# Kernel tuning notes

Hardware: AMD Instinct MI355X
Metric: run time of the kernel (lower is better)

The kernel has to match this reference:

```python
import jax, jax.numpy as jnp
import numpy as np
import math

DIM = 1536
N_HEADS = 12
HEAD_DIM = DIM // N_HEADS  # 128
C = HEAD_DIM // 2          # 64 complex rotation channels
CT = C - 2 * (C // 3)      # 22 temporal channels
CH = C // 3                # 21 height channels
CW = C // 3                # 21 width channels
F, H, W = 3, 30, 52        # video latent grid -> S = 4680
S = F * H * W
B = 1
EPS = 1e-6
NEG = -1e30


def _rope_angles(max_pos, sizes):
    # Wan-style rope_params per axis: theta_j = 10000^(-j/m) for m complex dims
    parts = []
    pos = jnp.arange(max_pos, dtype=jnp.float32)
    for m in sizes:
        inv = 10000.0 ** (-jnp.arange(m, dtype=jnp.float32) / m)
        parts.append(pos[:, None] * inv[None, :])
    return jnp.concatenate(parts, axis=-1)  # [max_pos, C]


def setup_inputs() -> dict:
    key = jax.random.key(0)
    ks = jax.random.split(key, 6)
    sc = 0.02
    inp = {
        'x': jax.random.normal(ks[0], (B, S, DIM), jnp.float32),
        'seq_lens': jnp.array([S], dtype=jnp.int32),
        'grid_sizes': jnp.array([[F, H, W]], dtype=jnp.int32),
        'freqs': _rope_angles(1024, [CT, CH, CW]),  # [1024, 64] rotation angles
        'Wq': jax.random.normal(ks[1], (DIM, DIM), jnp.float32) * sc,
        'bq': jnp.zeros((DIM,), jnp.float32),
        'Wk': jax.random.normal(ks[2], (DIM, DIM), jnp.float32) * sc,
        'bk': jnp.zeros((DIM,), jnp.float32),
        'Wv': jax.random.normal(ks[3], (DIM, DIM), jnp.float32) * sc,
        'bv': jnp.zeros((DIM,), jnp.float32),
        'Wo': jax.random.normal(ks[4], (DIM, DIM), jnp.float32) * sc,
        'bo': jnp.zeros((DIM,), jnp.float32),
        'gq': jnp.ones((DIM,), jnp.float32),
        'gk': jnp.ones((DIM,), jnp.float32),
    }
    return inp


def _rmsnorm(x, g):
    return x * jax.lax.rsqrt(jnp.mean(x * x, axis=-1, keepdims=True) + EPS) * g


def _apply_rope(x, grid_sizes, freqs):
    # x: [B, S, n, d]; rotate consecutive pairs by 3D (t,h,w) factorized angles.
    b, s, n, d = x.shape
    f = grid_sizes[0, 0]
    h = grid_sizes[0, 1]
    w = grid_sizes[0, 2]
    pos = jnp.arange(s)
    t_idx = pos // (h * w)
    y_idx = (pos % (h * w)) // w
    x_idx = pos % w
    ang = jnp.concatenate([
        freqs[t_idx, :CT],
        freqs[y_idx, CT:CT + CH],
        freqs[x_idx, CT + CH:],
    ], axis=-1)  # [S, C]
    cos = jnp.cos(ang)[None, :, None, :]  # [1, S, 1, C]
    sin = jnp.sin(ang)[None, :, None, :]
    xp = x.reshape(b, s, n, d // 2, 2)
    xr, xi = xp[..., 0], xp[..., 1]
    out_r = xr * cos - xi * sin
    out_i = xr * sin + xi * cos
    return jnp.stack([out_r, out_i], axis=-1).reshape(b, s, n, d)


def reference(x, seq_lens, grid_sizes, freqs, Wq, bq, Wk, bk, Wv, bv, Wo, bo, gq, gk):
    b, s, _ = x.shape
    n, d = N_HEADS, HEAD_DIM
    q = _rmsnorm(x @ Wq.T + bq, gq).reshape(b, s, n, d)
    k = _rmsnorm(x @ Wk.T + bk, gk).reshape(b, s, n, d)
    v = (x @ Wv.T + bv).reshape(b, s, n, d)

    rq = _apply_rope(q, grid_sizes, freqs)
    rk = _apply_rope(k, grid_sizes, freqs)

    # frame-level block-causal mask (block_mask in the original flex_attention)
    frame_seqlen = grid_sizes[0, 1] * grid_sizes[0, 2]
    frame_id = jnp.arange(s) // frame_seqlen
    allowed = frame_id[:, None] >= frame_id[None, :]  # [S, S]

    scale = 1.0 / math.sqrt(d)
    scores = jnp.einsum('bqnd,bknd->bnqk', rq, rk) * scale
    scores = jnp.where(allowed[None, None], scores, NEG)
    attn = jax.nn.softmax(scores, axis=-1)
    out = jnp.einsum('bnqk,bknd->bqnd', attn, v).reshape(b, s, n * d)
    return out @ Wo.T + bo
```

## Files before the change

### kernel.cpp

```cpp
#include <hip/hip_runtime.h>
#include <hip/hip_bf16.h>
#include <math.h>
#include <stdint.h>

#define S_LEN 4680
#define DIMSZ 1536
#define NH    12
#define HD    128
#define FRAME 1560
#define SP    4736
#define SQPAD 4736

typedef _Float16 f16;
typedef _Float16 f16x8 __attribute__((ext_vector_type(8)));
typedef _Float16 f16x4 __attribute__((ext_vector_type(4)));
typedef __fp16   fp16x2 __attribute__((ext_vector_type(2)));
typedef float    f32x4 __attribute__((ext_vector_type(4)));

__device__ __forceinline__ void async16(const void* g, void* l) {
    __builtin_amdgcn_global_load_lds((const __attribute__((address_space(1))) void*)g,
                                     (__attribute__((address_space(3))) void*)l, 16, 0, 0);
}

union PkCast { fp16x2 v; int i; };
union FragCast { int w[4]; f16x8 v; };

__global__ __launch_bounds__(256) void cast_f32_f16(const float* __restrict__ src,
                                                    f16* __restrict__ dst, int n4) {
    int i = blockIdx.x * 256 + threadIdx.x;
    if (i < n4) {
        float4 v = ((const float4*)src)[i];
        f16x4 h;
        h[0] = (f16)v.x; h[1] = (f16)v.y; h[2] = (f16)v.z; h[3] = (f16)v.w;
        ((f16x4*)dst)[i] = h;
    }
}

__global__ __launch_bounds__(256) void gemm_lds(const f16* __restrict__ A,
                                                const f16* __restrict__ B,
                                                const float* __restrict__ bias,
                                                float* __restrict__ C) {
    __shared__ __align__(16) f16 Al[128 * 64];
    __shared__ __align__(16) f16 Bl[128 * 64];
    int tid = threadIdx.x;
    int lane = tid & 63, wv = tid >> 6;
    int l16 = lane & 15, quad = lane >> 4;
    int wr = (wv >> 1) * 64, wc = (wv & 1) * 64;
    int m0 = blockIdx.x * 128, n0 = blockIdx.y * 128;

    f32x4 acc[4][4] = {};

    for (int kb = 0; kb < DIMSZ; kb += 64) {
        __syncthreads();
#pragma unroll
        for (int j = 0; j < 4; j++) {
            int s = j * 256 + wv * 64 + lane;
            int r = s >> 3, cc = s & 7;
            const f16* src = A + (size_t)min(m0 + r, S_LEN - 1) * DIMSZ + kb + ((cc ^ (r & 7)) << 3);
            async16(src, (char*)Al + (j * 4096 + wv * 1024));
        }
#pragma unroll
        for (int j = 0; j < 4; j++) {
            int s = j * 256 + wv * 64 + lane;
            int r = s >> 3, cc = s & 7;
            const f16* src = B + (size_t)(n0 + r) * DIMSZ + kb + ((cc ^ (r & 7)) << 3);
            async16(src, (char*)Bl + (j * 4096 + wv * 1024));
        }
        __builtin_amdgcn_s_waitcnt(0x0f70);
        __syncthreads();

#pragma unroll
        for (int kc = 0; kc < 2; kc++) {
            f16x8 af[4], bf[4];
#pragma unroll
            for (int i = 0; i < 4; i++) {
                int ar = wr + i * 16 + l16;
                af[i] = *(const f16x8*)((const char*)Al + ar * 128 + (((kc * 4 + quad) ^ (ar & 7)) << 4));
                int br = wc + i * 16 + l16;
                bf[i] = *(const f16x8*)((const char*)Bl + br * 128 + (((kc * 4 + quad) ^ (br & 7)) << 4));
            }
#pragma unroll
            for (int mi = 0; mi < 4; mi++)
#pragma unroll
                for (int ni = 0; ni < 4; ni++)
                    acc[mi][ni] = __builtin_amdgcn_mfma_f32_16x16x32_f16(af[mi], bf[ni], acc[mi][ni], 0, 0, 0);
        }
    }

#pragma unroll
    for (int mi = 0; mi < 4; mi++)
#pragma unroll
        for (int ni = 0; ni < 4; ni++) {
            int col = n0 + wc + ni * 16 + l16;
            float bv = bias[col];
#pragma unroll
            for (int r = 0; r < 4; r++) {
                int row = m0 + wr + mi * 16 + quad * 4 + r;
                if (row < S_LEN) C[(size_t)row * DIMSZ + col] = acc[mi][ni][r] + bv;
            }
        }
}

__global__ __launch_bounds__(256) void gemm_ldsvt(const f16* __restrict__ A,
                                                  const f16* __restrict__ B,
                                                  const float* __restrict__ bias,
                                                  f16* __restrict__ Vt) {
    __shared__ __align__(16) f16 Al[128 * 64];
    __shared__ __align__(16) f16 Bl[128 * 64];
    int tid = threadIdx.x;
    int lane = tid & 63, wv = tid >> 6;
    int l16 = lane & 15, quad = lane >> 4;
    int wr = (wv >> 1) * 64, wc = (wv & 1) * 64;
    int m0 = blockIdx.x * 128, n0 = blockIdx.y * 128;

    f32x4 acc[4][4] = {};

    for (int kb = 0; kb < DIMSZ; kb += 64) {
        __syncthreads();
#pragma unroll
        for (int j = 0; j < 4; j++) {
            int s = j * 256 + wv * 64 + lane;
            int r = s >> 3, cc = s & 7;
            const f16* src = A + (size_t)min(m0 + r, S_LEN - 1) * DIMSZ + kb + ((cc ^ (r & 7)) << 3);
            async16(src, (char*)Al + (j * 4096 + wv * 1024));
        }
#pragma unroll
        for (int j = 0; j < 4; j++) {
            int s = j * 256 + wv * 64 + lane;
            int r = s >> 3, cc = s & 7;
            const f16* src = B + (size_t)(n0 + r) * DIMSZ + kb + ((cc ^ (r & 7)) << 3);
            async16(src, (char*)Bl + (j * 4096 + wv * 1024));
        }
        __builtin_amdgcn_s_waitcnt(0x0f70);
        __syncthreads();

#pragma unroll
        for (int kc = 0; kc < 2; kc++) {
            f16x8 af[4], bf[4];
#pragma unroll
            for (int i = 0; i < 4; i++) {
                int ar = wr + i * 16 + l16;
                af[i] = *(const f16x8*)((const char*)Al + ar * 128 + (((kc * 4 + quad) ^ (ar & 7)) << 4));
                int br = wc + i * 16 + l16;
                bf[i] = *(const f16x8*)((const char*)Bl + br * 128 + (((kc * 4 + quad) ^ (br & 7)) << 4));
            }
#pragma unroll
            for (int mi = 0; mi < 4; mi++)
#pragma unroll
                for (int ni = 0; ni < 4; ni++)
                    acc[mi][ni] = __builtin_amdgcn_mfma_f32_16x16x32_f16(af[mi], bf[ni], acc[mi][ni], 0, 0, 0);
        }
    }

#pragma unroll
    for (int mi = 0; mi < 4; mi++)
#pragma unroll
        for (int ni = 0; ni < 4; ni++) {
            int col  = n0 + wc + ni * 16 + l16;
            int base = m0 + wr + mi * 16 + quad * 4;
            if (base < S_LEN) {
                float bv = bias[col];
                f16x4 h;
#pragma unroll
                for (int r = 0; r < 4; r++) h[r] = (f16)(acc[mi][ni][r] + bv);
                *(f16x4*)(Vt + (size_t)col * SP + base) = h;
            }
        }
}

__global__ __launch_bounds__(256) void norm_rope(const float* __restrict__ pre,
                                                 const float* __restrict__ g,
                                                 const float* __restrict__ freqs,
                                                 f16* __restrict__ dst) {
    int s = blockIdx.x;
    int t = threadIdx.x;
    const float* row = pre + (size_t)s * DIMSZ;

    float v[6];
    float ss = 0.f;
#pragma unroll
    for (int i = 0; i < 6; i++) { v[i] = row[t * 6 + i]; ss += v[i] * v[i]; }
#pragma unroll
    for (int off = 32; off; off >>= 1) ss += __shfl_xor(ss, off);
    __shared__ float red[4];
    if ((t & 63) == 0) red[t >> 6] = ss;
    __syncthreads();
    float tot = red[0] + red[1] + red[2] + red[3];
    float rms = rsqrtf(tot * (1.0f / DIMSZ) + 1e-6f);

    int tpos = s / FRAME;
    int rem  = s % FRAME;
    int ypos = rem / 52;
    int xpos = s % 52;

#pragma unroll
    for (int u = 0; u < 3; u++) {
        int c = t * 6 + u * 2;
        int head = c >> 7;
        int d = c & 127;
        int j = d >> 1;
        int idx = (j < 22) ? tpos : ((j < 43) ? ypos : xpos);
        float ang = freqs[idx * 64 + j];
        float sn, cs;
        __sincosf(ang, &sn, &cs);
        float vr = v[u * 2]     * rms * g[c];
        float vi = v[u * 2 + 1] * rms * g[c + 1];
        f16* o = dst + ((size_t)head * S_LEN + s) * HD + d;
        o[0] = (f16)(vr * cs - vi * sn);
        o[1] = (f16)(vr * sn + vi * cs);
    }
}

__global__ __launch_bounds__(256) void attn_part(const f16* __restrict__ Q,
                                                 const f16* __restrict__ K,
                                                 const f16* __restrict__ Vt,
                                                 f16* __restrict__ Opart,
                                                 float* __restrict__ lpart) {
    int bx = blockIdx.x, head = blockIdx.y;
    int t, c;
    if (bx < 12)      { t = bx;                 c = 0; }
    else if (bx < 36) { t = 12 + (bx - 12) / 2; c = (bx - 12) & 1; }
    else              { t = 24 + (bx - 36) / 3; c = (bx - 36) % 3; }

    int tid = threadIdx.x;
    int lane = tid & 63, wv = tid >> 6;
    int l16 = lane & 15, quad = lane >> 4;
    int qbase = t * 128 + wv * 32;

    __shared__ __align__(16) char smem[128 * 136 * 2];
    f16* Klds = (f16*)smem;
    f16* Vlds = (f16*)(smem + 16384);
    f16* obuf = (f16*)smem;

    const f16* Qh = Q  + (size_t)head * S_LEN * HD;
    const f16* Kh = K  + (size_t)head * S_LEN * HD;
    const f16* Vh = Vt + (size_t)head * HD * SP;

    f16x8 aq[2][4];
    int lim[2];
    int c0 = c * FRAME, cend = c0 + FRAME;
#pragma unroll
    for (int qt = 0; qt < 2; qt++) {
        int qr = min(qbase + qt * 16 + l16, S_LEN - 1);
        const f16* Qp = Qh + (size_t)qr * HD + quad * 8;
#pragma unroll
        for (int kc = 0; kc < 4; kc++)
            aq[qt][kc] = (*(const f16x8*)(Qp + kc * 32)) * (f16)0.08838834764831845f;
        lim[qt] = min((qr / FRAME + 1) * FRAME, cend);
    }

    f32x4 oacc[2][8] = {};
    float lp[2] = {0.f, 0.f};

    int losel = ((quad & 1) * 2) * 16 + l16;
    int hisel = losel + 16;
    bool upper = (quad & 2) != 0;

    for (int it = 0; it < 25; it++) {
        int kb = c0 + it * 64;
        __syncthreads();
#pragma unroll
        for (int i = 0; i < 4; i++) {
            int s  = i * 4 + wv;
            int ch = s * 64 + lane;
            int row = ch >> 4;
            int cc  = (ch & 15) ^ (row & 15);
            async16(Kh + (size_t)min(kb + row, S_LEN - 1) * HD + cc * 8,
                    (char*)Klds + s * 1024);
        }
#pragma unroll
        for (int i = 0; i < 4; i++) {
            int s  = i * 4 + wv;
            int ch = s * 64 + lane;
            int vr = ch >> 3;
            int cc = (ch & 7) ^ (vr & 7);
            async16(Vh + (size_t)vr * SP + kb + cc * 8,
                    (char*)Vlds + s * 1024);
        }
        __builtin_amdgcn_s_waitcnt(0x0f70);
        __syncthreads();

        f32x4 sc[2][4] = {};
#pragma unroll
        for (int kt = 0; kt < 4; kt++) {
            int krow = kt * 16 + l16;
#pragma unroll
            for (int kc = 0; kc < 4; kc++) {
                f16x8 kf = *(const f16x8*)((const char*)Klds + krow * 256 +
                                           (((kc * 4 + quad) ^ l16) << 4));
                sc[0][kt] = __builtin_amdgcn_mfma_f32_16x16x32_f16(kf, aq[0][kc], sc[0][kt], 0, 0, 0);
                sc[1][kt] = __builtin_amdgcn_mfma_f32_16x16x32_f16(kf, aq[1][kc], sc[1][kt], 0, 0, 0);
            }
        }

        int dw[2][4][2];
#pragma unroll
        for (int qt = 0; qt < 2; qt++)
#pragma unroll
            for (int kt = 0; kt < 4; kt++) {
                int keyb = kb + kt * 16 + quad * 4;
#pragma unroll
                for (int u = 0; u < 2; u++) {
                    float p0 = (keyb + 2 * u     < lim[qt]) ? __expf(sc[qt][kt][2 * u])     : 0.f;
                    float p1 = (keyb + 2 * u + 1 < lim[qt]) ? __expf(sc[qt][kt][2 * u + 1]) : 0.f;
                    lp[qt] += p0 + p1;
                    PkCast pk; pk.v = __builtin_amdgcn_cvt_pkrtz(p0, p1);
                    dw[qt][kt][u] = pk.i;
                }
            }

        f16x8 pb[2][2];
#pragma unroll
        for (int qt = 0; qt < 2; qt++)
#pragma unroll
            for (int b0 = 0; b0 < 2; b0++) {
                int a0 = __shfl(dw[qt][2 * b0][0],     losel);
                int a1 = __shfl(dw[qt][2 * b0][1],     losel);
                int a2 = __shfl(dw[qt][2 * b0][0],     hisel);
                int a3 = __shfl(dw[qt][2 * b0][1],     hisel);
                int b0w = __shfl(dw[qt][2 * b0 + 1][0], losel);
                int b1w = __shfl(dw[qt][2 * b0 + 1][1], losel);
                int b2w = __shfl(dw[qt][2 * b0 + 1][0], hisel);
                int b3w = __shfl(dw[qt][2 * b0 + 1][1], hisel);
                FragCast fc;
                fc.w[0] = upper ? b0w : a0;
                fc.w[1] = upper ? b1w : a1;
                fc.w[2] = upper ? b2w : a2;
                fc.w[3] = upper ? b3w : a3;
                pb[qt][b0] = fc.v;
            }

#pragma unroll
        for (int vn = 0; vn < 8; vn++) {
            int vrow = vn * 16 + l16;
            f16x8 v0 = *(const f16x8*)((const char*)Vlds + vrow * 128 + (((quad)     ^ (vrow & 7)) << 4));
            f16x8 v1 = *(const f16x8*)((const char*)Vlds + vrow * 128 + (((4 + quad) ^ (vrow & 7)) << 4));
#pragma unroll
            for (int qt = 0; qt < 2; qt++) {
                oacc[qt][vn] = __builtin_amdgcn_mfma_f32_16x16x32_f16(v0, pb[qt][0], oacc[qt][vn], 0, 0, 0);
                oacc[qt][vn] = __builtin_amdgcn_mfma_f32_16x16x32_f16(v1, pb[qt][1], oacc[qt][vn], 0, 0, 0);
            }
        }
    }

    float inv[2];
#pragma unroll
    for (int qt = 0; qt < 2; qt++) {
        float l = lp[qt];
        l += __shfl_xor(l, 16);
        l += __shfl_xor(l, 32);
        lp[qt] = l;
        inv[qt] = 1.f / l;
    }

    __syncthreads();
#pragma unroll
    for (int qt = 0; qt < 2; qt++) {
        int qloc = wv * 32 + qt * 16 + l16;
#pragma unroll
        for (int vn = 0; vn < 8; vn++) {
            f16x4 h;
#pragma unroll
            for (int r = 0; r < 4; r++) h[r] = (f16)(oacc[qt][vn][r] * inv[qt]);
            *(f16x4*)(obuf + qloc * 136 + vn * 16 + quad * 4) = h;
        }
        if (quad == 0) {
            int row = qbase + qt * 16 + l16;
            lpart[(size_t)(c * NH + head) * SQPAD + row] = lp[qt];
        }
    }
    __syncthreads();

    int qloc = tid >> 1, hh = tid & 1;
    size_t obase = ((size_t)(c * NH + head) * SQPAD + t * 128 + qloc) * HD;
#pragma unroll
    for (int p = 0; p < 8; p++) {
        int d = hh * 64 + p * 8;
        f16x8 o = *(const f16x8*)(obuf + qloc * 136 + d);
        *(f16x8*)(Opart + obase + d) = o;
    }
}

__global__ __launch_bounds__(256) void combine(const f16* __restrict__ Opart,
                                               const float* __restrict__ lpart,
                                               f16* __restrict__ AO) {
    int gid = blockIdx.x * 256 + threadIdx.x;
    if (gid >= S_LEN * NH * 16) return;
    int dc = gid & 15;
    int head = (gid >> 4) % NH;
    int q = gid / (NH * 16);
    int tt = q >> 7;
    int qlast = min(tt * 128 + 127, S_LEN - 1);
    int nf = qlast / FRAME + 1;

    float sum[8] = {};
    float ls = 0.f;
    for (int c = 0; c < nf; c++) {
        float l = lpart[(size_t)(c * NH + head) * SQPAD + q];
        if (l > 0.f) {
            f16x8 o = *(const f16x8*)(Opart + ((size_t)(c * NH + head) * SQPAD + q) * HD + dc * 8);
#pragma unroll
            for (int j = 0; j < 8; j++) sum[j] += (float)o[j] * l;
            ls += l;
        }
    }
    float invl = 1.f / ls;
    f16x8 r;
#pragma unroll
    for (int j = 0; j < 8; j++) r[j] = (f16)(sum[j] * invl);
    *(f16x8*)(AO + (size_t)q * DIMSZ + head * HD + dc * 8) = r;
}

extern "C" void kernel_launch(void* const* d_in, const int* in_sizes, int n_in,
                              void* d_out, int out_size, void* d_ws, size_t ws_size,
                              hipStream_t stream) {
    const float* x     = (const float*)d_in[0];
    const float* freqs = (const float*)d_in[3];
    const float* Wq = (const float*)d_in[4];
    const float* bq = (const float*)d_in[5];
    const float* Wk = (const float*)d_in[6];
    const float* bk = (const float*)d_in[7];
    const float* Wv = (const float*)d_in[8];
    const float* bv = (const float*)d_in[9];
    const float* Wo = (const float*)d_in[10];
    const float* bo = (const float*)d_in[11];
    const float* gq = (const float*)d_in[12];
    const float* gk = (const float*)d_in[13];
    float* out = (float*)d_out;

    char* ws = (char*)d_ws;
    const size_t SZ_XH = (size_t)S_LEN * DIMSZ * 2;
    const size_t SZ_W  = (size_t)DIMSZ * DIMSZ * 2;
    const size_t SZ_VT = (size_t)NH * HD * SP * 2;
    const size_t SZ_OP = (size_t)3 * NH * SQPAD * HD * 2;

    size_t off = 0;
    f16* xh  = (f16*)(ws + off); off += SZ_XH;
    f16* wqh = (f16*)(ws + off); off += SZ_W;
    f16* wkh = (f16*)(ws + off); off += SZ_W;
    f16* wvh = (f16*)(ws + off); off += SZ_W;
    f16* woh = (f16*)(ws + off); off += SZ_W;
    f16* Qb  = (f16*)(ws + off); off += SZ_XH;
    f16* Kb  = (f16*)(ws + off); off += SZ_XH;
    f16* Vtb = (f16*)(ws + off); off += SZ_VT;
    f16* AO  = (f16*)(ws + off); off += SZ_XH;
    float* pre   = (float*)(ws + off);
    f16*   Opart = (f16*)(ws + off);
    float* lpart = (float*)(ws + off + SZ_OP);

    const int nX4 = (S_LEN * DIMSZ) / 4;
    const int nW4 = (DIMSZ * DIMSZ) / 4;

    cast_f32_f16<<<nX4 / 256, 256, 0, stream>>>(x,  xh,  nX4);
    cast_f32_f16<<<nW4 / 256, 256, 0, stream>>>(Wq, wqh, nW4);
    cast_f32_f16<<<nW4 / 256, 256, 0, stream>>>(Wk, wkh, nW4);
    cast_f32_f16<<<nW4 / 256, 256, 0, stream>>>(Wv, wvh, nW4);
    cast_f32_f16<<<nW4 / 256, 256, 0, stream>>>(Wo, woh, nW4);

    dim3 ggrid(37, 12);

    gemm_lds<<<ggrid, 256, 0, stream>>>(xh, wqh, bq, pre);
    norm_rope<<<S_LEN, 256, 0, stream>>>(pre, gq, freqs, Qb);
    gemm_lds<<<ggrid, 256, 0, stream>>>(xh, wkh, bk, pre);
    norm_rope<<<S_LEN, 256, 0, stream>>>(pre, gk, freqs, Kb);
    gemm_ldsvt<<<ggrid, 256, 0, stream>>>(xh, wvh, bv, Vtb);

    attn_part<<<dim3(75, 12), 256, 0, stream>>>(Qb, Kb, Vtb, Opart, lpart);
    combine<<<(S_LEN * NH * 16) / 256, 256, 0, stream>>>(Opart, lpart, AO);

    gemm_lds<<<ggrid, 256, 0, stream>>>(AO, woh, bo, out);
}
```

Before: 567.1 us.

## Fuse QKV projections, panelize Q/K/V layout, and rewrite attention with 32x32 MFMA

Merges the five cast kernels into one launch and the three QKV GEMMs into a single z-batched launch. Pre-norm Q/K are stored in fp16 instead of fp32, and Q/K/V are written in a 64-row panel layout so attention can load contiguous 16 KB tiles. The attention kernel now uses 128-thread blocks with 32x32x16 MFMA, permlane32 swaps for the P fragment, and masking only on boundary tiles. This cuts launch count, intermediate traffic and attention instruction overhead, at the cost of extra fp16 rounding before RMSNorm and a larger, more complex kernel.

```diff
diff --git a/kernel.cpp b/kernel.cpp
--- a/kernel.cpp
+++ b/kernel.cpp
@@ -8,14 +8,18 @@
 #define NH    12
 #define HD    128
 #define FRAME 1560
-#define SP    4736
+#define NGRP  74
 #define SQPAD 4736
+#define PANH  (NGRP * 8192)
 
 typedef _Float16 f16;
 typedef _Float16 f16x8 __attribute__((ext_vector_type(8)));
 typedef _Float16 f16x4 __attribute__((ext_vector_type(4)));
+typedef _Float16 f16x2 __attribute__((ext_vector_type(2)));
 typedef __fp16   fp16x2 __attribute__((ext_vector_type(2)));
-typedef float    f32x4 __attribute__((ext_vector_type(4)));
+typedef float    f32x4  __attribute__((ext_vector_type(4)));
+typedef float    f32x16 __attribute__((ext_vector_type(16)));
+typedef int      v2i    __attribute__((ext_vector_type(2)));
 
 __device__ __forceinline__ void async16(const void* g, void* l) {
     __builtin_amdgcn_global_load_lds((const __attribute__((address_space(1))) void*)g,
@@ -25,15 +29,390 @@
 union PkCast { fp16x2 v; int i; };
 union FragCast { int w[4]; f16x8 v; };
 
-__global__ __launch_bounds__(256) void cast_f32_f16(const float* __restrict__ src,
-                                                    f16* __restrict__ dst, int n4) {
+__global__ __launch_bounds__(256) void cast_all(const float* __restrict__ x,
+                                                const float* __restrict__ wq,
+                                                const float* __restrict__ wk,
+                                                const float* __restrict__ wv,
+                                                const float* __restrict__ wo,
+                                                f16* __restrict__ xh,
+                                                f16* __restrict__ wh) {
+    int y = blockIdx.y;
     int i = blockIdx.x * 256 + threadIdx.x;
-    if (i < n4) {
-        float4 v = ((const float4*)src)[i];
-        f16x4 h;
-        h[0] = (f16)v.x; h[1] = (f16)v.y; h[2] = (f16)v.z; h[3] = (f16)v.w;
-        ((f16x4*)dst)[i] = h;
-    }
+    if (y == 0) {
+        if (i < (S_LEN * DIMSZ) / 4) {
+            float4 v = ((const float4*)x)[i];
+            f16x4 h; h[0]=(f16)v.x; h[1]=(f16)v.y; h[2]=(f16)v.z; h[3]=(f16)v.w;
+            ((f16x4*)xh)[i] = h;
+        }
+    } else {
+        const int nW4 = (DIMSZ * DIMSZ) / 4;
+        if (i < nW4) {
+            const float* src = (y==1)?wq:(y==2)?wk:(y==3)?wv:wo;
+            float4 v = ((const float4*)src)[i];
+            f16x4 h; h[0]=(f16)v.x; h[1]=(f16)v.y; h[2]=(f16)v.z; h[3]=(f16)v.w;
+            ((f16x4*)wh)[(size_t)(y-1)*nW4 + i] = h;
+        }
+    }
+}
+
+__global__ __launch_bounds__(256) void gemm_qkv(const f16* __restrict__ A,
+                                                const f16* __restrict__ Bq,
+                                                const f16* __restrict__ Bk,
+                                                const f16* __restrict__ Bv,
+                                                const float* __restrict__ bq,
+                                                const float* __restrict__ bk,
+                                                const float* __restrict__ bv,
+                                                f16* __restrict__ preq,
+                                                f16* __restrict__ prek,
+                                                f16* __restrict__ vtp) {
+    int z = blockIdx.z;
+    const f16* B = (z==0) ? Bq : (z==1) ? Bk : Bv;
+    const float* bias = (z==0) ? bq : (z==1) ? bk : bv;
+
+    __shared__ __align__(16) f16 Al[128 * 64];
+    __shared__ __align__(16) f16 Bl[128 * 64];
+    int tid = threadIdx.x;
+    int lane = tid & 63, wv = tid >> 6;
+    int l16 = lane & 15, quad = lane >> 4;
+    int wr = (wv >> 1) * 64, wc = (wv & 1) * 64;
+    int m0 = blockIdx.x * 128, n0 = blockIdx.y * 128;
+
+    f32x4 acc[4][4] = {};
+
+    for (int kb = 0; kb < DIMSZ; kb += 64) {
+        __syncthreads();
+#pragma unroll
+        for (int j = 0; j < 4; j++) {
+            int s = j * 256 + wv * 64 + lane;
+            int r = s >> 3, cc = s & 7;
+            const f16* src = A + (size_t)min(m0 + r, S_LEN - 1) * DIMSZ + kb + ((cc ^ (r & 7)) << 3);
+            async16(src, (char*)Al + (j * 4096 + wv * 1024));
+        }
+#pragma unroll
+        for (int j = 0; j < 4; j++) {
+            int s = j * 256 + wv * 64 + lane;
+            int r = s >> 3, cc = s & 7;
+            const f16* src = B + (size_t)(n0 + r) * DIMSZ + kb + ((cc ^ (r & 7)) << 3);
+            async16(src, (char*)Bl + (j * 4096 + wv * 1024));
+        }
+        __builtin_amdgcn_s_waitcnt(0x0f70);
+        __syncthreads();
+
+#pragma unroll
+        for (int kc = 0; kc < 2; kc++) {
+            f16x8 af[4], bf[4];
+#pragma unroll
+            for (int i = 0; i < 4; i++) {
+                int ar = wr + i * 16 + l16;
+                af[i] = *(const f16x8*)((const char*)Al + ar * 128 + (((kc * 4 + quad) ^ (ar & 7)) << 4));
+                int br = wc + i * 16 + l16;
+                bf[i] = *(const f16x8*)((const char*)Bl + br * 128 + (((kc * 4 + quad) ^ (br & 7)) << 4));
+            }
+#pragma unroll
+            for (int mi = 0; mi < 4; mi++)
+#pragma unroll
+                for (int ni = 0; ni < 4; ni++)
+                    acc[mi][ni] = __builtin_amdgcn_mfma_f32_16x16x32_f16(af[mi], bf[ni], acc[mi][ni], 0, 0, 0);
+        }
+    }
+
+    if (z < 2) {
+        f16* C = (z == 0) ? preq : prek;
+#pragma unroll
+        for (int mi = 0; mi < 4; mi++)
+#pragma unroll
+            for (int ni = 0; ni < 4; ni++) {
+                int col = n0 + wc + ni * 16 + l16;
+                float bv_ = bias[col];
+#pragma unroll
+                for (int r = 0; r < 4; r++) {
+                    int row = m0 + wr + mi * 16 + quad * 4 + r;
+                    if (row < S_LEN) C[(size_t)row * DIMSZ + col] = (f16)(acc[mi][ni][r] + bv_);
+                }
+            }
+    } else {
+#pragma unroll
+        for (int mi = 0; mi < 4; mi++)
+#pragma unroll
+            for (int ni = 0; ni < 4; ni++) {
+                int col  = n0 + wc + ni * 16 + l16;
+                int vhead = col >> 7, d = col & 127;
+                int base = m0 + wr + mi * 16 + quad * 4;
+                if (base < S_LEN) {
+                    float bv_ = bias[col];
+                    f16x4 h;
+#pragma unroll
+                    for (int r = 0; r < 4; r++) h[r] = (f16)(acc[mi][ni][r] + bv_);
+                    size_t off = (size_t)vhead * PANH + (size_t)(base >> 6) * 8192
+                               + ((base >> 3) & 7) * 1024 + d * 8 + (base & 7);
+                    *(f16x4*)(vtp + off) = h;
+                }
+            }
+    }
+}
+
+__global__ __launch_bounds__(256) void norm_rope(const f16* __restrict__ preq,
+                                                 const f16* __restrict__ prek,
+                                                 const float* __restrict__ gq,
+                                                 const float* __restrict__ gk,
+                                                 const float* __restrict__ freqs,
+                                                 f16* __restrict__ Qp,
+                                                 f16* __restrict__ Kp) {
+    int s = blockIdx.x, which = blockIdx.y;
+    int t = threadIdx.x;
+    const f16* pre = which ? prek : preq;
+    const float* g = which ? gk : gq;
+    f16* dst = which ? Kp : Qp;
+    const f16* row = pre + (size_t)s * DIMSZ + t * 6;
+
+    float v[6];
+    float ss = 0.f;
+#pragma unroll
+    for (int i = 0; i < 3; i++) {
+        f16x2 hp = *(const f16x2*)(row + 2 * i);
+        v[2*i] = (float)hp[0]; v[2*i+1] = (float)hp[1];
+        ss += v[2*i]*v[2*i] + v[2*i+1]*v[2*i+1];
+    }
+#pragma unroll
+    for (int off = 32; off; off >>= 1) ss += __shfl_xor(ss, off);
+    __shared__ float red[4];
+    if ((t & 63) == 0) red[t >> 6] = ss;
+    __syncthreads();
+    float tot = red[0] + red[1] + red[2] + red[3];
+    float rms = rsqrtf(tot * (1.0f / DIMSZ) + 1e-6f);
+
+    int tpos = s / FRAME;
+    int rem  = s % FRAME;
+    int ypos = rem / 52;
+    int xpos = s % 52;
+
+#pragma unroll
+    for (int u = 0; u < 3; u++) {
+        int c = t * 6 + u * 2;
+        int head = c >> 7;
+        int d = c & 127;
+        int j = d >> 1;
+        int idx = (j < 22) ? tpos : ((j < 43) ? ypos : xpos);
+        float ang = freqs[idx * 64 + j];
+        float sn, cs;
+        __sincosf(ang, &sn, &cs);
+        float vr = v[u * 2]     * rms * g[c];
+        float vi = v[u * 2 + 1] * rms * g[c + 1];
+        f16* o = dst + (size_t)head * PANH + (size_t)(s >> 6) * 8192
+               + (d >> 3) * 512 + (s & 63) * 8 + (d & 7);
+        o[0] = (f16)(vr * cs - vi * sn);
+        o[1] = (f16)(vr * sn + vi * cs);
+    }
+}
+
+__global__ __launch_bounds__(128, 2) void attn_part(const f16* __restrict__ Qp,
+                                                    const f16* __restrict__ Kp,
+                                                    const f16* __restrict__ Vp,
+                                                    f16* __restrict__ Opart,
+                                                    float* __restrict__ lpart) {
+    int bx = blockIdx.x, head = blockIdx.y;
+    int t, c;
+    if (bx < 12)      { t = bx;                 c = 0; }
+    else if (bx < 36) { t = 12 + (bx - 12) / 2; c = (bx - 12) & 1; }
+    else              { t = 24 + (bx - 36) / 3; c = (bx - 36) % 3; }
+
+    int qlast = min(t * 128 + 127, S_LEN - 1);
+    int nc    = qlast / FRAME + 1;
+    int kvend = nc * FRAME; if (kvend > S_LEN) kvend = S_LEN;
+    int nG    = (kvend + 63) >> 6;
+    int g0 = (c * nG) / nc, g1 = ((c + 1) * nG) / nc;
+    int limB = ((t * 128) / FRAME + 1) * FRAME;
+
+    int tid = threadIdx.x, lane = tid & 63, wv = tid >> 6;
+    int l31 = lane & 31, lh = lane >> 5;
+    int qw = t * 128 + wv * 64;
+
+    __shared__ __align__(16) char smem[32768];
+    const char* smc = smem;
+
+    const f16* Qg = Qp + ((size_t)head * NGRP + (qw >> 6)) * 8192;
+    f16x8 bqf[2][8];
+#pragma unroll
+    for (int nt = 0; nt < 2; nt++)
+#pragma unroll
+        for (int ks = 0; ks < 8; ks++) {
+            f16x8 vq = *(const f16x8*)(Qg + (2 * ks + lh) * 512 + (l31 + 32 * nt) * 8);
+            bqf[nt][ks] = vq * (f16)0.08838834764831845f;
+        }
+
+    int lim[2];
+#pragma unroll
+    for (int nt = 0; nt < 2; nt++) {
+        int q = qw + l31 + 32 * nt;
+        lim[nt] = (q / FRAME + 1) * FRAME;
+    }
+
+    f32x16 oacc[4][2] = {};
+    float lp[2] = {0.f, 0.f};
+
+    int koff = lh * 1024 + l31 * 16;
+    int voff = lh * 2048 + l31 * 16;
+
+    for (int g = g0; g < g1; g++) {
+        int kb = g * 64;
+        __syncthreads();
+        const f16* Kg = Kp + ((size_t)head * NGRP + g) * 8192;
+        const f16* Vg = Vp + ((size_t)head * NGRP + g) * 8192;
+#pragma unroll
+        for (int i = 0; i < 8; i++) {
+            int s = i * 2 + wv;
+            async16(Kg + s * 512 + lane * 8, (char*)smem + s * 1024 + lane * 16);
+        }
+#pragma unroll
+        for (int i = 0; i < 8; i++) {
+            int s = i * 2 + wv;
+            async16(Vg + s * 512 + lane * 8, (char*)smem + 16384 + s * 1024 + lane * 16);
+        }
+        __builtin_amdgcn_s_waitcnt(0x0f70);
+        __syncthreads();
+
+        bool domask = (kb + 64 > limB);
+
+#pragma unroll
+        for (int kt = 0; kt < 2; kt++) {
+            f32x16 sc0 = {}, sc1 = {};
+#pragma unroll
+            for (int h = 0; h < 2; h++) {
+                f16x8 ka[4];
+#pragma unroll
+                for (int i = 0; i < 4; i++)
+                    ka[i] = *(const f16x8*)(smc + koff + (h * 4 + i) * 2048 + kt * 512);
+#pragma unroll
+                for (int i = 0; i < 4; i++) {
+                    sc0 = __builtin_amdgcn_mfma_f32_32x32x16_f16(ka[i], bqf[0][h*4+i], sc0, 0, 0, 0);
+                    sc1 = __builtin_amdgcn_mfma_f32_32x32x16_f16(ka[i], bqf[1][h*4+i], sc1, 0, 0, 0);
+                }
+            }
+
+            int w[2][8];
+            int keyb = kb + kt * 32 + 4 * lh;
+#pragma unroll
+            for (int nt = 0; nt < 2; nt++) {
+#pragma unroll
+                for (int p = 0; p < 8; p++) {
+                    const int r0 = 2 * p;
+                    float s0 = (nt == 0) ? sc0[r0]     : sc1[r0];
+                    float s1 = (nt == 0) ? sc0[r0 + 1] : sc1[r0 + 1];
+                    if (domask) {
+                        int k0 = keyb + (r0 & 3) + 8 * (r0 >> 2);
+                        if (k0     >= lim[nt]) s0 = -1e30f;
+                        if (k0 + 1 >= lim[nt]) s1 = -1e30f;
+                    }
+                    float p0 = __expf(s0), p1 = __expf(s1);
+                    lp[nt] += p0 + p1;
+                    PkCast pk; pk.v = __builtin_amdgcn_cvt_pkrtz(p0, p1);
+                    w[nt][p] = pk.i;
+                }
+            }
+
+            f16x8 pb[2][2];
+#pragma unroll
+            for (int nt = 0; nt < 2; nt++)
+#pragma unroll
+                for (int ks = 0; ks < 2; ks++) {
+                    FragCast fc;
+#if __has_builtin(__builtin_amdgcn_permlane32_swap)
+                    v2i r02 = __builtin_amdgcn_permlane32_swap(w[nt][4*ks+0], w[nt][4*ks+2], false, false);
+                    v2i r13 = __builtin_amdgcn_permlane32_swap(w[nt][4*ks+1], w[nt][4*ks+3], false, false);
+                    fc.w[0] = r02.x; fc.w[1] = r13.x; fc.w[2] = r02.y; fc.w[3] = r13.y;
+#else
+                    int w0 = w[nt][4*ks], w1 = w[nt][4*ks+1], w2 = w[nt][4*ks+2], w3 = w[nt][4*ks+3];
+                    fc.w[0] = lh ? __shfl_xor(w2, 32) : w0;
+                    fc.w[1] = lh ? __shfl_xor(w3, 32) : w1;
+                    fc.w[2] = lh ? w2 : __shfl_xor(w0, 32);
+                    fc.w[3] = lh ? w3 : __shfl_xor(w1, 32);
+#endif
+                    pb[nt][ks] = fc.v;
+                }
+
+#pragma unroll
+            for (int mt = 0; mt < 4; mt++)
+#pragma unroll
+                for (int ks = 0; ks < 2; ks++) {
+                    f16x8 va = *(const f16x8*)(smc + 16384 + voff + kt * 8192 + ks * 4096 + mt * 512);
+                    oacc[mt][0] = __builtin_amdgcn_mfma_f32_32x32x16_f16(va, pb[0][ks], oacc[mt][0], 0, 0, 0);
+                    oacc[mt][1] = __builtin_amdgcn_mfma_f32_32x32x16_f16(va, pb[1][ks], oacc[mt][1], 0, 0, 0);
+                }
+        }
+    }
+
+    float lt[2], linv[2];
+#pragma unroll
+    for (int nt = 0; nt < 2; nt++) {
+        float l = lp[nt] + __shfl_xor(lp[nt], 32);
+        lt[nt] = l;
+        linv[nt] = (l > 0.f) ? 1.f / l : 0.f;
+    }
+
+    __syncthreads();
+    char* ob = (char*)smem + wv * 16384;
+#pragma unroll
+    for (int mt = 0; mt < 4; mt++)
+#pragma unroll
+        for (int nt = 0; nt < 2; nt++) {
+            int qloc = l31 + 32 * nt;
+#pragma unroll
+            for (int g4 = 0; g4 < 4; g4++) {
+                f16x4 hv;
+#pragma unroll
+                for (int r = 0; r < 4; r++) hv[r] = (f16)(oacc[mt][nt][g4 * 4 + r] * linv[nt]);
+                int c16 = g4 + 4 * mt;
+                *(f16x4*)(ob + qloc * 256 + ((c16 ^ (qloc & 7)) << 4) + lh * 8) = hv;
+            }
+        }
+    __syncthreads();
+
+    size_t obase = ((size_t)(c * NH + head) * SQPAD + qw) * HD;
+#pragma unroll
+    for (int a = 0; a < 4; a++)
+#pragma unroll
+        for (int b = 0; b < 4; b++) {
+            int qloc = a * 16 + (lane >> 2);
+            int c16  = (lane & 3) + 4 * b;
+            f16x8 vv = *(const f16x8*)(ob + qloc * 256 + ((c16 ^ (qloc & 7)) << 4));
+            *(f16x8*)(Opart + obase + (size_t)qloc * HD + c16 * 8) = vv;
+        }
+
+    if (lane < 32) {
+        size_t lbase = (size_t)(c * NH + head) * SQPAD + qw;
+        lpart[lbase + l31]      = lt[0];
+        lpart[lbase + l31 + 32] = lt[1];
+    }
+}
+
+__global__ __launch_bounds__(256) void combine(const f16* __restrict__ Opart,
+                                               const float* __restrict__ lpart,
+                                               f16* __restrict__ AO) {
+    int gid = blockIdx.x * 256 + threadIdx.x;
+    if (gid >= S_LEN * NH * 16) return;
+    int dc = gid & 15;
+    int head = (gid >> 4) % NH;
+    int q = gid / (NH * 16);
+    int tt = q >> 7;
+    int qlast = min(tt * 128 + 127, S_LEN - 1);
+    int nf = qlast / FRAME + 1;
+
+    float sum[8] = {};
+    float ls = 0.f;
+    for (int c = 0; c < nf; c++) {
+        float l = lpart[(size_t)(c * NH + head) * SQPAD + q];
+        if (l > 0.f) {
+            f16x8 o = *(const f16x8*)(Opart + ((size_t)(c * NH + head) * SQPAD + q) * HD + dc * 8);
+#pragma unroll
+            for (int j = 0; j < 8; j++) sum[j] += (float)o[j] * l;
+            ls += l;
+        }
+    }
+    float invl = 1.f / ls;
+    f16x8 r;
+#pragma unroll
+    for (int j = 0; j < 8; j++) r[j] = (f16)(sum[j] * invl);
+    *(f16x8*)(AO + (size_t)q * DIMSZ + head * HD + dc * 8) = r;
 }
 
 __global__ __launch_bounds__(256) void gemm_lds(const f16* __restrict__ A,
@@ -99,316 +478,6 @@
                 if (row < S_LEN) C[(size_t)row * DIMSZ + col] = acc[mi][ni][r] + bv;
             }
         }
-}
-
-__global__ __launch_bounds__(256) void gemm_ldsvt(const f16* __restrict__ A,
-                                                  const f16* __restrict__ B,
-                                                  const float* __restrict__ bias,
-                                                  f16* __restrict__ Vt) {
-    __shared__ __align__(16) f16 Al[128 * 64];
-    __shared__ __align__(16) f16 Bl[128 * 64];
-    int tid = threadIdx.x;
-    int lane = tid & 63, wv = tid >> 6;
-    int l16 = lane & 15, quad = lane >> 4;
-    int wr = (wv >> 1) * 64, wc = (wv & 1) * 64;
-    int m0 = blockIdx.x * 128, n0 = blockIdx.y * 128;
-
-    f32x4 acc[4][4] = {};
-
-    for (int kb = 0; kb < DIMSZ; kb += 64) {
-        __syncthreads();
-#pragma unroll
-        for (int j = 0; j < 4; j++) {
-            int s = j * 256 + wv * 64 + lane;
-            int r = s >> 3, cc = s & 7;
-            const f16* src = A + (size_t)min(m0 + r, S_LEN - 1) * DIMSZ + kb + ((cc ^ (r & 7)) << 3);
-            async16(src, (char*)Al + (j * 4096 + wv * 1024));
-        }
-#pragma unroll
-        for (int j = 0; j < 4; j++) {
-            int s = j * 256 + wv * 64 + lane;
-            int r = s >> 3, cc = s & 7;
-            const f16* src = B + (size_t)(n0 + r) * DIMSZ + kb + ((cc ^ (r & 7)) << 3);
-            async16(src, (char*)Bl + (j * 4096 + wv * 1024));
-        }
-        __builtin_amdgcn_s_waitcnt(0x0f70);
-        __syncthreads();
-
-#pragma unroll
-        for (int kc = 0; kc < 2; kc++) {
-            f16x8 af[4], bf[4];
-#pragma unroll
-            for (int i = 0; i < 4; i++) {
-                int ar = wr + i * 16 + l16;
-                af[i] = *(const f16x8*)((const char*)Al + ar * 128 + (((kc * 4 + quad) ^ (ar & 7)) << 4));
-                int br = wc + i * 16 + l16;
-                bf[i] = *(const f16x8*)((const char*)Bl + br * 128 + (((kc * 4 + quad) ^ (br & 7)) << 4));
-            }
-#pragma unroll
-            for (int mi = 0; mi < 4; mi++)
-#pragma unroll
-                for (int ni = 0; ni < 4; ni++)
-                    acc[mi][ni] = __builtin_amdgcn_mfma_f32_16x16x32_f16(af[mi], bf[ni], acc[mi][ni], 0, 0, 0);
-        }
-    }
-
-#pragma unroll
-    for (int mi = 0; mi < 4; mi++)
-#pragma unroll
-        for (int ni = 0; ni < 4; ni++) {
-            int col  = n0 + wc + ni * 16 + l16;
-            int base = m0 + wr + mi * 16 + quad * 4;
-            if (base < S_LEN) {
-                float bv = bias[col];
-                f16x4 h;
-#pragma unroll
-                for (int r = 0; r < 4; r++) h[r] = (f16)(acc[mi][ni][r] + bv);
-                *(f16x4*)(Vt + (size_t)col * SP + base) = h;
-            }
-        }
-}
-
-__global__ __launch_bounds__(256) void norm_rope(const float* __restrict__ pre,
-                                                 const float* __restrict__ g,
-                                                 const float* __restrict__ freqs,
-                                                 f16* __restrict__ dst) {
-    int s = blockIdx.x;
-    int t = threadIdx.x;
-    const float* row = pre + (size_t)s * DIMSZ;
-
-    float v[6];
-    float ss = 0.f;
-#pragma unroll
-    for (int i = 0; i < 6; i++) { v[i] = row[t * 6 + i]; ss += v[i] * v[i]; }
-#pragma unroll
-    for (int off = 32; off; off >>= 1) ss += __shfl_xor(ss, off);
-    __shared__ float red[4];
-    if ((t & 63) == 0) red[t >> 6] = ss;
-    __syncthreads();
-    float tot = red[0] + red[1] + red[2] + red[3];
-    float rms = rsqrtf(tot * (1.0f / DIMSZ) + 1e-6f);
-
-    int tpos = s / FRAME;
-    int rem  = s % FRAME;
-    int ypos = rem / 52;
-    int xpos = s % 52;
-
-#pragma unroll
-    for (int u = 0; u < 3; u++) {
-        int c = t * 6 + u * 2;
-        int head = c >> 7;
-        int d = c & 127;
-        int j = d >> 1;
-        int idx = (j < 22) ? tpos : ((j < 43) ? ypos : xpos);
-        float ang = freqs[idx * 64 + j];
-        float sn, cs;
-        __sincosf(ang, &sn, &cs);
-        float vr = v[u * 2]     * rms * g[c];
-        float vi = v[u * 2 + 1] * rms * g[c + 1];
-        f16* o = dst + ((size_t)head * S_LEN + s) * HD + d;
-        o[0] = (f16)(vr * cs - vi * sn);
-        o[1] = (f16)(vr * sn + vi * cs);
-    }
-}
-
-__global__ __launch_bounds__(256) void attn_part(const f16* __restrict__ Q,
-                                                 const f16* __restrict__ K,
-                                                 const f16* __restrict__ Vt,
-                                                 f16* __restrict__ Opart,
-                                                 float* __restrict__ lpart) {
-    int bx = blockIdx.x, head = blockIdx.y;
-    int t, c;
-    if (bx < 12)      { t = bx;                 c = 0; }
-    else if (bx < 36) { t = 12 + (bx - 12) / 2; c = (bx - 12) & 1; }
-    else              { t = 24 + (bx - 36) / 3; c = (bx - 36) % 3; }
-
-    int tid = threadIdx.x;
-    int lane = tid & 63, wv = tid >> 6;
-    int l16 = lane & 15, quad = lane >> 4;
-    int qbase = t * 128 + wv * 32;
-
-    __shared__ __align__(16) char smem[128 * 136 * 2];
-    f16* Klds = (f16*)smem;
-    f16* Vlds = (f16*)(smem + 16384);
-    f16* obuf = (f16*)smem;
-
-    const f16* Qh = Q  + (size_t)head * S_LEN * HD;
-    const f16* Kh = K  + (size_t)head * S_LEN * HD;
-    const f16* Vh = Vt + (size_t)head * HD * SP;
-
-    f16x8 aq[2][4];
-    int lim[2];
-    int c0 = c * FRAME, cend = c0 + FRAME;
-#pragma unroll
-    for (int qt = 0; qt < 2; qt++) {
-        int qr = min(qbase + qt * 16 + l16, S_LEN - 1);
-        const f16* Qp = Qh + (size_t)qr * HD + quad * 8;
-#pragma unroll
-        for (int kc = 0; kc < 4; kc++)
-            aq[qt][kc] = (*(const f16x8*)(Qp + kc * 32)) * (f16)0.08838834764831845f;
-        lim[qt] = min((qr / FRAME + 1) * FRAME, cend);
-    }
-
-    f32x4 oacc[2][8] = {};
-    float lp[2] = {0.f, 0.f};
-
-    int losel = ((quad & 1) * 2) * 16 + l16;
-    int hisel = losel + 16;
-    bool upper = (quad & 2) != 0;
-
-    for (int it = 0; it < 25; it++) {
-        int kb = c0 + it * 64;
-        __syncthreads();
-#pragma unroll
-        for (int i = 0; i < 4; i++) {
-            int s  = i * 4 + wv;
-            int ch = s * 64 + lane;
-            int row = ch >> 4;
-            int cc  = (ch & 15) ^ (row & 15);
-            async16(Kh + (size_t)min(kb + row, S_LEN - 1) * HD + cc * 8,
-                    (char*)Klds + s * 1024);
-        }
-#pragma unroll
-        for (int i = 0; i < 4; i++) {
-            int s  = i * 4 + wv;
-            int ch = s * 64 + lane;
-            int vr = ch >> 3;
-            int cc = (ch & 7) ^ (vr & 7);
-            async16(Vh + (size_t)vr * SP + kb + cc * 8,
-                    (char*)Vlds + s * 1024);
-        }
-        __builtin_amdgcn_s_waitcnt(0x0f70);
-        __syncthreads();
-
-        f32x4 sc[2][4] = {};
-#pragma unroll
-        for (int kt = 0; kt < 4; kt++) {
-            int krow = kt * 16 + l16;
-#pragma unroll
-            for (int kc = 0; kc < 4; kc++) {
-                f16x8 kf = *(const f16x8*)((const char*)Klds + krow * 256 +
-                                           (((kc * 4 + quad) ^ l16) << 4));
-                sc[0][kt] = __builtin_amdgcn_mfma_f32_16x16x32_f16(kf, aq[0][kc], sc[0][kt], 0, 0, 0);
-                sc[1][kt] = __builtin_amdgcn_mfma_f32_16x16x32_f16(kf, aq[1][kc], sc[1][kt], 0, 0, 0);
-            }
-        }
-
-        int dw[2][4][2];
-#pragma unroll
-        for (int qt = 0; qt < 2; qt++)
-#pragma unroll
-            for (int kt = 0; kt < 4; kt++) {
-                int keyb = kb + kt * 16 + quad * 4;
-#pragma unroll
-                for (int u = 0; u < 2; u++) {
-                    float p0 = (keyb + 2 * u     < lim[qt]) ? __expf(sc[qt][kt][2 * u])     : 0.f;
-                    float p1 = (keyb + 2 * u + 1 < lim[qt]) ? __expf(sc[qt][kt][2 * u + 1]) : 0.f;
-                    lp[qt] += p0 + p1;
-                    PkCast pk; pk.v = __builtin_amdgcn_cvt_pkrtz(p0, p1);
-                    dw[qt][kt][u] = pk.i;
-                }
-            }
-
-        f16x8 pb[2][2];
-#pragma unroll
-        for (int qt = 0; qt < 2; qt++)
-#pragma unroll
-            for (int b0 = 0; b0 < 2; b0++) {
-                int a0 = __shfl(dw[qt][2 * b0][0],     losel);
-                int a1 = __shfl(dw[qt][2 * b0][1],     losel);
-                int a2 = __shfl(dw[qt][2 * b0][0],     hisel);
-                int a3 = __shfl(dw[qt][2 * b0][1],     hisel);
-                int b0w = __shfl(dw[qt][2 * b0 + 1][0], losel);
-                int b1w = __shfl(dw[qt][2 * b0 + 1][1], losel);
-                int b2w = __shfl(dw[qt][2 * b0 + 1][0], hisel);
-                int b3w = __shfl(dw[qt][2 * b0 + 1][1], hisel);
-                FragCast fc;
-                fc.w[0] = upper ? b0w : a0;
-                fc.w[1] = upper ? b1w : a1;
-                fc.w[2] = upper ? b2w : a2;
-                fc.w[3] = upper ? b3w : a3;
-                pb[qt][b0] = fc.v;
-            }
-
-#pragma unroll
-        for (int vn = 0; vn < 8; vn++) {
-            int vrow = vn * 16 + l16;
-            f16x8 v0 = *(const f16x8*)((const char*)Vlds + vrow * 128 + (((quad)     ^ (vrow & 7)) << 4));
-            f16x8 v1 = *(const f16x8*)((const char*)Vlds + vrow * 128 + (((4 + quad) ^ (vrow & 7)) << 4));
-#pragma unroll
-            for (int qt = 0; qt < 2; qt++) {
-                oacc[qt][vn] = __builtin_amdgcn_mfma_f32_16x16x32_f16(v0, pb[qt][0], oacc[qt][vn], 0, 0, 0);
-                oacc[qt][vn] = __builtin_amdgcn_mfma_f32_16x16x32_f16(v1, pb[qt][1], oacc[qt][vn], 0, 0, 0);
-            }
-        }
-    }
-
-    float inv[2];
-#pragma unroll
-    for (int qt = 0; qt < 2; qt++) {
-        float l = lp[qt];
-        l += __shfl_xor(l, 16);
-        l += __shfl_xor(l, 32);
-        lp[qt] = l;
-        inv[qt] = 1.f / l;
-    }
-
-    __syncthreads();
-#pragma unroll
-    for (int qt = 0; qt < 2; qt++) {
-        int qloc = wv * 32 + qt * 16 + l16;
-#pragma unroll
-        for (int vn = 0; vn < 8; vn++) {
-            f16x4 h;
-#pragma unroll
-            for (int r = 0; r < 4; r++) h[r] = (f16)(oacc[qt][vn][r] * inv[qt]);
-            *(f16x4*)(obuf + qloc * 136 + vn * 16 + quad * 4) = h;
-        }
-        if (quad == 0) {
-            int row = qbase + qt * 16 + l16;
-            lpart[(size_t)(c * NH + head) * SQPAD + row] = lp[qt];
-        }
-    }
-    __syncthreads();
-
-    int qloc = tid >> 1, hh = tid & 1;
-    size_t obase = ((size_t)(c * NH + head) * SQPAD + t * 128 + qloc) * HD;
-#pragma unroll
-    for (int p = 0; p < 8; p++) {
-        int d = hh * 64 + p * 8;
-        f16x8 o = *(const f16x8*)(obuf + qloc * 136 + d);
-        *(f16x8*)(Opart + obase + d) = o;
-    }
-}
-
-__global__ __launch_bounds__(256) void combine(const f16* __restrict__ Opart,
-                                               const float* __restrict__ lpart,
-                                               f16* __restrict__ AO) {
-    int gid = blockIdx.x * 256 + threadIdx.x;
-    if (gid >= S_LEN * NH * 16) return;
-    int dc = gid & 15;
-    int head = (gid >> 4) % NH;
-    int q = gid / (NH * 16);
-    int tt = q >> 7;
-    int qlast = min(tt * 128 + 127, S_LEN - 1);
-    int nf = qlast / FRAME + 1;
-
-    float sum[8] = {};
-    float ls = 0.f;
-    for (int c = 0; c < nf; c++) {
-        float l = lpart[(size_t)(c * NH + head) * SQPAD + q];
-        if (l > 0.f) {
-            f16x8 o = *(const f16x8*)(Opart + ((size_t)(c * NH + head) * SQPAD + q) * HD + dc * 8);
-#pragma unroll
-            for (int j = 0; j < 8; j++) sum[j] += (float)o[j] * l;
-            ls += l;
-        }
-    }
-    float invl = 1.f / ls;
-    f16x8 r;
-#pragma unroll
-    for (int j = 0; j < 8; j++) r[j] = (f16)(sum[j] * invl);
-    *(f16x8*)(AO + (size_t)q * DIMSZ + head * HD + dc * 8) = r;
 }
 
 extern "C" void kernel_launch(void* const* d_in, const int* in_sizes, int n_in,
@@ -429,44 +498,35 @@
     float* out = (float*)d_out;
 
     char* ws = (char*)d_ws;
-    const size_t SZ_XH = (size_t)S_LEN * DIMSZ * 2;
-    const size_t SZ_W  = (size_t)DIMSZ * DIMSZ * 2;
-    const size_t SZ_VT = (size_t)NH * HD * SP * 2;
-    const size_t SZ_OP = (size_t)3 * NH * SQPAD * HD * 2;
+    const size_t SZ_XH  = (size_t)S_LEN * DIMSZ * 2;
+    const size_t SZ_W   = (size_t)DIMSZ * DIMSZ * 2;
+    const size_t SZ_PAN = (size_t)NH * PANH * 2;
+    const size_t SZ_OP  = (size_t)3 * NH * SQPAD * HD * 2;
 
     size_t off = 0;
-    f16* xh  = (f16*)(ws + off); off += SZ_XH;
-    f16* wqh = (f16*)(ws + off); off += SZ_W;
-    f16* wkh = (f16*)(ws + off); off += SZ_W;
-    f16* wvh = (f16*)(ws + off); off += SZ_W;
-    f16* woh = (f16*)(ws + off); off += SZ_W;
-    f16* Qb  = (f16*)(ws + off); off += SZ_XH;
-    f16* Kb  = (f16*)(ws + off); off += SZ_XH;
-    f16* Vtb = (f16*)(ws + off); off += SZ_VT;
-    f16* AO  = (f16*)(ws + off); off += SZ_XH;
-    float* pre   = (float*)(ws + off);
+    f16* xh   = (f16*)(ws + off); off += SZ_XH;
+    f16* wqh  = (f16*)(ws + off); off += 4 * SZ_W;
+    f16* wkh  = wqh + (size_t)DIMSZ * DIMSZ;
+    f16* wvh  = wkh + (size_t)DIMSZ * DIMSZ;
+    f16* woh  = wvh + (size_t)DIMSZ * DIMSZ;
+    f16* Qpan = (f16*)(ws + off); off += SZ_PAN;
+    f16* Kpan = (f16*)(ws + off); off += SZ_PAN;
+    f16* Vpan = (f16*)(ws + off); off += SZ_PAN;
+    f16* AO   = (f16*)(ws + off); off += SZ_XH;
+    f16*   preq  = (f16*)(ws + off);
+    f16*   prek  = preq + (size_t)S_LEN * DIMSZ;
     f16*   Opart = (f16*)(ws + off);
     float* lpart = (float*)(ws + off + SZ_OP);
 
-    const int nX4 = (S_LEN * DIMSZ) / 4;
-    const int nW4 = (DIMSZ * DIMSZ) / 4;
-
-    cast_f32_f16<<<nX4 / 256, 256, 0, stream>>>(x,  xh,  nX4);
-    cast_f32_f16<<<nW4 / 256, 256, 0, stream>>>(Wq, wqh, nW4);
-    cast_f32_f16<<<nW4 / 256, 256, 0, stream>>>(Wk, wkh, nW4);
-    cast_f32_f16<<<nW4 / 256, 256, 0, stream>>>(Wv, wvh, nW4);
-    cast_f32_f16<<<nW4 / 256, 256, 0, stream>>>(Wo, woh, nW4);
-
-    dim3 ggrid(37, 12);
-
-    gemm_lds<<<ggrid, 256, 0, stream>>>(xh, wqh, bq, pre);
-    norm_rope<<<S_LEN, 256, 0, stream>>>(pre, gq, freqs, Qb);
-    gemm_lds<<<ggrid, 256, 0, stream>>>(xh, wkh, bk, pre);
-    norm_rope<<<S_LEN, 256, 0, stream>>>(pre, gk, freqs, Kb);
-    gemm_ldsvt<<<ggrid, 256, 0, stream>>>(xh, wvh, bv, Vtb);
-
-    attn_part<<<dim3(75, 12), 256, 0, stream>>>(Qb, Kb, Vtb, Opart, lpart);
+    cast_all<<<dim3(7020, 5), 256, 0, stream>>>(x, Wq, Wk, Wv, Wo, xh, wqh);
+
+    gemm_qkv<<<dim3(37, 12, 3), 256, 0, stream>>>(xh, wqh, wkh, wvh, bq, bk, bv,
+                                                  preq, prek, Vpan);
+
+    norm_rope<<<dim3(S_LEN, 2), 256, 0, stream>>>(preq, prek, gq, gk, freqs, Qpan, Kpan);
+
+    attn_part<<<dim3(75, 12), 128, 0, stream>>>(Qpan, Kpan, Vpan, Opart, lpart);
     combine<<<(S_LEN * NH * 16) / 256, 256, 0, stream>>>(Opart, lpart, AO);
 
-    gemm_lds<<<ggrid, 256, 0, stream>>>(AO, woh, bo, out);
-}
+    gemm_lds<<<dim3(37, 12), 256, 0, stream>>>(AO, woh, bo, out);
+}
```

New measurement: 505.6 us. 1.12x faster.
